# Kernel tuning notes

Hardware: AMD Instinct MI355X
Metric: run time of the kernel (lower is better)

Reference implementation:

```python
import jax, jax.numpy as jnp
import numpy as np

EPS = 1e-5

def _bn(x, gamma, beta):
    # x: [B, N, C]; training-mode BatchNorm1d over (B, N)
    mu = jnp.mean(x, axis=(0, 1))
    var = jnp.var(x, axis=(0, 1))
    return (x - mu) * jax.lax.rsqrt(var + EPS) * gamma + beta


def setup_inputs() -> dict:
    key = jax.random.key(0)
    ks = jax.random.split(key, 32)
    B, N = 16, 8192
    enc_dim, mem_dim = 1024, 1024
    feat_dim = enc_dim + mem_dim  # 2048
    n_points = 2048
    s = 0.02
    d = {
        'partial': jax.random.normal(ks[0], (B, N, 3), jnp.float32),
        # first_conv: Conv1d(3,128,1) + BN(128) + ReLU + Conv1d(128,256,1)
        'W1': jax.random.normal(ks[1], (128, 3), jnp.float32) * s,
        'b1': jnp.zeros((128,), jnp.float32),
        'g1': jnp.ones((128,), jnp.float32),
        'be1': jnp.zeros((128,), jnp.float32),
        'W2': jax.random.normal(ks[2], (256, 128), jnp.float32) * s,
        'b2': jnp.zeros((256,), jnp.float32),
        # second_conv: Conv1d(512,512,1) + BN(512) + ReLU + Conv1d(512,enc_dim,1)
        'W3': jax.random.normal(ks[3], (512, 512), jnp.float32) * s,
        'b3': jnp.zeros((512,), jnp.float32),
        'g2': jnp.ones((512,), jnp.float32),
        'be2': jnp.zeros((512,), jnp.float32),
        'W4': jax.random.normal(ks[4], (enc_dim, 512), jnp.float32) * s,
        'b4': jnp.zeros((enc_dim,), jnp.float32),
        # MemoryModule gates: Linear(enc_dim, mem_dim) x4 + memory param
        'Wf': jax.random.normal(ks[5], (mem_dim, enc_dim), jnp.float32) * s,
        'bf': jnp.zeros((mem_dim,), jnp.float32),
        'Wi': jax.random.normal(ks[6], (mem_dim, enc_dim), jnp.float32) * s,
        'bi': jnp.zeros((mem_dim,), jnp.float32),
        'Wo': jax.random.normal(ks[7], (mem_dim, enc_dim), jnp.float32) * s,
        'bo': jnp.zeros((mem_dim,), jnp.float32),
        'Wc': jax.random.normal(ks[8], (mem_dim, enc_dim), jnp.float32) * s,
        'bc': jnp.zeros((mem_dim,), jnp.float32),
        'mem': jax.random.normal(ks[9], (1, mem_dim), jnp.float32),
        # Decoder MLP: feat_dim->2048->2048->2048->3*n_points
        'D1w': jax.random.normal(ks[10], (2048, feat_dim), jnp.float32) * s,
        'D1b': jnp.zeros((2048,), jnp.float32),
        'D2w': jax.random.normal(ks[11], (2048, 2048), jnp.float32) * s,
        'D2b': jnp.zeros((2048,), jnp.float32),
        'D3w': jax.random.normal(ks[12], (2048, 2048), jnp.float32) * s,
        'D3b': jnp.zeros((2048,), jnp.float32),
        'D4w': jax.random.normal(ks[13], (3 * n_points, 2048), jnp.float32) * s,
        'D4b': jnp.zeros((3 * n_points,), jnp.float32),
    }
    return d


def reference(partial, W1, b1, g1, be1, W2, b2, W3, b3, g2, be2, W4, b4,
              Wf, bf, Wi, bi, Wo, bo, Wc, bc, mem,
              D1w, D1b, D2w, D2b, D3w, D3b, D4w, D4b):
    B, N, _ = partial.shape
    # --- Encoder first_conv (pointwise convs == per-point linear) ---
    f = jnp.einsum('bnc,dc->bnd', partial, W1) + b1          # [B,N,128]
    f = jax.nn.relu(_bn(f, g1, be1))
    f = jnp.einsum('bnc,dc->bnd', f, W2) + b2                # [B,N,256]
    fg = jnp.max(f, axis=1, keepdims=True)                   # [B,1,256]
    f = jnp.concatenate([jnp.broadcast_to(fg, (B, N, 256)), f], axis=-1)  # [B,N,512]
    # --- second_conv ---
    f = jnp.einsum('bnc,dc->bnd', f, W3) + b3                # [B,N,512]
    f = jax.nn.relu(_bn(f, g2, be2))
    f = jnp.einsum('bnc,dc->bnd', f, W4) + b4                # [B,N,enc_dim]
    feat_global = jnp.max(f, axis=1)                         # [B,enc_dim]
    # --- MemoryModule (flag=False: memory not updated) ---
    fgate = jax.nn.sigmoid(feat_global @ Wf.T + bf)
    igate = jax.nn.sigmoid(feat_global @ Wi.T + bi)
    ogate = jax.nn.sigmoid(feat_global @ Wo.T + bo)
    cand = jnp.tanh(feat_global @ Wc.T + bc)
    mem_b = jnp.broadcast_to(mem, fgate.shape)
    h = ogate * jnp.tanh(fgate * mem_b + igate * cand)       # [B,mem_dim]
    feat = jnp.concatenate([feat_global, h], axis=1)         # [B,feat_dim]
    # --- Decoder MLP ---
    z = jax.nn.relu(feat @ D1w.T + D1b)
    z = jax.nn.relu(z @ D2w.T + D2b)
    z = jax.nn.relu(z @ D3w.T + D3b)
    z = z @ D4w.T + D4b                                      # [B, 3*n_points]
    return z.reshape(B, -1, 3)
```

## Files before the change

kernel.cpp:

```cpp
#include <hip/hip_runtime.h>
#include <hip/hip_bf16.h>

typedef __bf16 v8bf __attribute__((ext_vector_type(8)));
typedef float  v4f  __attribute__((ext_vector_type(4)));

#define NPTS (16*8192)
#define RPB  8192

#define GLOAD_LDS16(g, l) __builtin_amdgcn_global_load_lds( \
    (const __attribute__((address_space(1))) void*)(g), \
    (__attribute__((address_space(3))) void*)(l), 16, 0, 0)

__device__ __forceinline__ unsigned fenc(float x){
    unsigned u = __float_as_uint(x);
    return (u & 0x80000000u) ? ~u : (u | 0x80000000u);
}
__device__ __forceinline__ float fdec(unsigned u){
    return __uint_as_float((u & 0x80000000u) ? (u ^ 0x80000000u) : ~u);
}

__device__ __forceinline__ v8bf bn_relu8(v8bf v, float4 s0, float4 s1, float4 h0, float4 h1){
    v8bf r;
    r[0] = (__bf16)fmaxf(fmaf((float)v[0], s0.x, h0.x), 0.f);
    r[1] = (__bf16)fmaxf(fmaf((float)v[1], s0.y, h0.y), 0.f);
    r[2] = (__bf16)fmaxf(fmaf((float)v[2], s0.z, h0.z), 0.f);
    r[3] = (__bf16)fmaxf(fmaf((float)v[3], s0.w, h0.w), 0.f);
    r[4] = (__bf16)fmaxf(fmaf((float)v[4], s1.x, h1.x), 0.f);
    r[5] = (__bf16)fmaxf(fmaf((float)v[5], s1.y, h1.y), 0.f);
    r[6] = (__bf16)fmaxf(fmaf((float)v[6], s1.z, h1.z), 0.f);
    r[7] = (__bf16)fmaxf(fmaf((float)v[7], s1.w, h1.w), 0.f);
    return r;
}

__global__ __launch_bounds__(256) void stats1_k(const float* __restrict__ P,
        const float* __restrict__ W1, const float* __restrict__ b1,
        float* __restrict__ gsum, float* __restrict__ gsumsq)
{
    int tid = threadIdx.x;
    int c = tid & 127, half = tid >> 7;
    float w0 = W1[c*3+0], w1 = W1[c*3+1], w2 = W1[c*3+2], bb = b1[c];
    float s = 0.f, s2 = 0.f;
    int base = blockIdx.x * 512 + half;
    for (int i = 0; i < 256; ++i) {
        int p = base + i*2;
        float x = P[p*3+0], y = P[p*3+1], z = P[p*3+2];
        float v = fmaf(w0,x, fmaf(w1,y, fmaf(w2,z, bb)));
        s += v; s2 = fmaf(v,v,s2);
    }
    __shared__ float ls[256], lq[256];
    ls[tid] = s; lq[tid] = s2;
    __syncthreads();
    if (half == 0) {
        atomicAdd(&gsum[c],   s  + ls[tid+128]);
        atomicAdd(&gsumsq[c], s2 + lq[tid+128]);
    }
}

__global__ void finalize_k(const float* __restrict__ gsum, const float* __restrict__ gsumsq,
        const float* __restrict__ gamma, const float* __restrict__ beta,
        float* __restrict__ scale, float* __restrict__ shift, int C, float invn)
{
    int c = blockIdx.x*blockDim.x + threadIdx.x;
    if (c >= C) return;
    float m   = gsum[c]*invn;
    float var = fmaxf(gsumsq[c]*invn - m*m, 0.f);
    float rs  = rsqrtf(var + 1e-5f);
    float sc  = gamma[c]*rs;
    scale[c] = sc;
    shift[c] = beta[c] - m*sc;
}

__global__ __launch_bounds__(256) void apply1_k(const float* __restrict__ P,
        const float* __restrict__ W1, const float* __restrict__ b1,
        const float* __restrict__ sc, const float* __restrict__ sh,
        __bf16* __restrict__ out)
{
    int tid = threadIdx.x;
    int c = tid & 127, ph = tid >> 7;
    float w0 = W1[c*3+0], w1 = W1[c*3+1], w2 = W1[c*3+2], bb = b1[c];
    float a = sc[c], b_ = sh[c];
    int base = blockIdx.x * 16 + ph;
    #pragma unroll
    for (int i = 0; i < 8; ++i) {
        int p = base + i*2;
        float x = P[p*3+0], y = P[p*3+1], z = P[p*3+2];
        float v = fmaf(w0,x, fmaf(w1,y, fmaf(w2,z, bb)));
        v = fmaxf(fmaf(v, a, b_), 0.f);
        out[(size_t)p*128 + c] = (__bf16)v;
    }
}

__global__ void cvt_k(const float* __restrict__ src, __bf16* __restrict__ dst,
                      int rows, int cols, int sstride, int coff)
{
    int i = blockIdx.x*256 + threadIdx.x;
    if (i >= rows*cols) return;
    int r = i / cols, c = i - r*cols;
    dst[i] = (__bf16)src[(size_t)r*sstride + coff + c];
}

template<bool STORE, bool DOMAX, bool STATS, bool BNA, int LOGNB>
__global__ __launch_bounds__(256, 2) void gemm_k(
        const __bf16* __restrict__ A, const __bf16* __restrict__ Bw,
        int K, int Nw,
        const float* __restrict__ bias, int bias_bstride,
        __bf16* __restrict__ Cout, unsigned* __restrict__ maxenc,
        float* __restrict__ gsum, float* __restrict__ gsq,
        const float* __restrict__ scA, const float* __restrict__ shA)
{
    __shared__ __bf16 As[128*64];
    __shared__ __bf16 Bs[256*64];
    __shared__ float lstat[2][2][256];

    const int tid  = threadIdx.x;
    const int lane = tid & 63;
    const int wave = tid >> 6;
    const int wr = wave >> 1, wc = wave & 1;
    const int nwg   = (int)gridDim.x;
    const int chunk = nwg >> 3;
    const int bi    = (int)blockIdx.x;
    const int li    = (bi & 7) * chunk + (bi >> 3);
    const int m0    = (li >> LOGNB) * 128;
    const int n0    = (li & ((1 << LOGNB) - 1)) * 256;
    const int srow = tid >> 3, sslot = tid & 7;
    const int lrow  = lane >> 3;
    const int swz   = ((lane & 7) ^ lrow) * 8;

    v4f acc[4][8];
    #pragma unroll
    for (int i=0;i<4;i++)
      #pragma unroll
      for (int j=0;j<8;j++) acc[i][j] = (v4f)(0.0f);

    v8bf ra[4];
    auto loadA_bn = [&](int kb){
        int kk = kb + sslot*8;
        float4 s0 = *(const float4*)(scA + kk);
        float4 s1 = *(const float4*)(scA + kk + 4);
        float4 h0 = *(const float4*)(shA + kk);
        float4 h1 = *(const float4*)(shA + kk + 4);
        #pragma unroll
        for (int i=0;i<4;i++){
            int r = i*32 + srow;
            v8bf v = *(const v8bf*)(A + (size_t)(m0+r)*K + kb + sslot*8);
            ra[i] = bn_relu8(v, s0, s1, h0, h1);
        }
    };
    auto stageB = [&](int kb){
        #pragma unroll
        for (int j=0;j<8;j++){
            int r0 = (wave*8 + j)*8;
            GLOAD_LDS16(Bw + (size_t)(n0 + r0 + lrow)*K + kb + swz, &Bs[r0*64]);
        }
    };
    auto stageA = [&](int kb){
        #pragma unroll
        for (int j=0;j<4;j++){
            int r0 = (wave*4 + j)*8;
            GLOAD_LDS16(A + (size_t)(m0 + r0 + lrow)*K + kb + swz, &As[r0*64]);
        }
    };

    if constexpr (BNA) loadA_bn(0);

    for (int k0 = 0; k0 < K; k0 += 64) {
        __syncthreads();
        stageB(k0);
        if constexpr (BNA) {
            #pragma unroll
            for (int i=0;i<4;i++){
                int r = i*32 + srow;
                *(v8bf*)(&As[r*64 + ((sslot ^ (r & 7))<<3)]) = ra[i];
            }
        } else {
            stageA(k0);
        }
        __syncthreads();
        if constexpr (BNA) { if (k0 + 64 < K) loadA_bn(k0 + 64); }
        #pragma unroll
        for (int kk = 0; kk < 2; ++kk) {
            v8bf af[4], bfr[8];
            #pragma unroll
            for (int i=0;i<4;i++){
                int arow = wr*64 + i*16 + (lane & 15);
                int sg = kk*4 + (lane >> 4);
                af[i] = *(const v8bf*)(&As[arow*64 + ((sg ^ (arow & 7))<<3)]);
            }
            #pragma unroll
            for (int j=0;j<8;j++){
                int brow = wc*128 + j*16 + (lane & 15);
                int sg = kk*4 + (lane >> 4);
                bfr[j] = *(const v8bf*)(&Bs[brow*64 + ((sg ^ (brow & 7))<<3)]);
            }
            #pragma unroll
            for (int i=0;i<4;i++)
              #pragma unroll
              for (int j=0;j<8;j++)
                acc[i][j] = __builtin_amdgcn_mfma_f32_16x16x32_bf16(af[i], bfr[j], acc[i][j], 0,0,0);
        }
    }

    const int b = m0 / RPB;
    const float* brow_ = bias + (size_t)b * bias_bstride;
    float colmax[8], csum[8], csq[8];
    #pragma unroll
    for (int j=0;j<8;j++){ colmax[j] = -3.402823466e38f; csum[j]=0.f; csq[j]=0.f; }

    #pragma unroll
    for (int i=0;i<4;i++){
        int rbase = m0 + wr*64 + i*16 + ((lane>>4)<<2);
        #pragma unroll
        for (int j=0;j<8;j++){
            int col = n0 + wc*128 + j*16 + (lane & 15);
            float bv = brow_[col];
            #pragma unroll
            for (int q=0;q<4;q++){
                float v = acc[i][j][q] + bv;
                if constexpr (STORE) Cout[(size_t)(rbase+q)*Nw + col] = (__bf16)v;
                if constexpr (DOMAX) colmax[j] = fmaxf(colmax[j], v);
                if constexpr (STATS) { csum[j] += v; csq[j] = fmaf(v,v,csq[j]); }
            }
        }
    }
    if constexpr (DOMAX) {
        #pragma unroll
        for (int j=0;j<8;j++){
            float v = colmax[j];
            v = fmaxf(v, __shfl_xor(v, 16));
            v = fmaxf(v, __shfl_xor(v, 32));
            if (lane < 16) {
                int col = n0 + wc*128 + j*16 + lane;
                atomicMax(&maxenc[(size_t)b*Nw + col], fenc(v));
            }
        }
    }
    if constexpr (STATS) {
        #pragma unroll
        for (int j=0;j<8;j++){
            float s = csum[j], q = csq[j];
            s += __shfl_xor(s, 16); s += __shfl_xor(s, 32);
            q += __shfl_xor(q, 16); q += __shfl_xor(q, 32);
            if (lane < 16) {
                int c = wc*128 + j*16 + lane;
                lstat[0][wr][c] = s;
                lstat[1][wr][c] = q;
            }
        }
        __syncthreads();
        if (tid < 256) {
            float s = lstat[0][0][tid] + lstat[0][1][tid];
            float q = lstat[1][0][tid] + lstat[1][1][tid];
            atomicAdd(&gsum[n0 + tid], s);
            atomicAdd(&gsq [n0 + tid], q);
        }
    }
}

__global__ __launch_bounds__(256) void bias3_k(const unsigned* __restrict__ fge,
        const float* __restrict__ W3, const float* __restrict__ b3,
        float* __restrict__ bias3)
{
    int b = blockIdx.x, tid = threadIdx.x;
    __shared__ float fg[256];
    fg[tid] = fdec(fge[b*256 + tid]);
    __syncthreads();
    for (int d = tid; d < 512; d += 256) {
        const float* wrow = W3 + (size_t)d*512;
        float s = b3[d];
        for (int c = 0; c < 256; c += 4) {
            s = fmaf(fg[c+0], wrow[c+0], s);
            s = fmaf(fg[c+1], wrow[c+1], s);
            s = fmaf(fg[c+2], wrow[c+2], s);
            s = fmaf(fg[c+3], wrow[c+3], s);
        }
        bias3[b*512 + d] = s;
    }
}

__global__ void decode_k(const unsigned* __restrict__ enc, float* __restrict__ feat)
{
    int i = blockIdx.x*256 + threadIdx.x;
    int b = i >> 10, c = i & 1023;
    feat[(size_t)b*2048 + c] = fdec(enc[i]);
}

__global__ __launch_bounds__(256) void gates_k(
        const float* __restrict__ Wf, const float* __restrict__ bfv,
        const float* __restrict__ Wi, const float* __restrict__ biv,
        const float* __restrict__ Wo, const float* __restrict__ bov,
        const float* __restrict__ Wc, const float* __restrict__ bcv,
        const float* __restrict__ memv, float* __restrict__ feat)
{
    int tid = threadIdx.x;
    int b = tid & 15;
    int j = blockIdx.x*16 + (tid >> 4);
    const float* x  = feat + (size_t)b*2048;
    const float* rf = Wf + (size_t)j*1024;
    const float* ri = Wi + (size_t)j*1024;
    const float* ro = Wo + (size_t)j*1024;
    const float* rc = Wc + (size_t)j*1024;
    float sf = bfv[j], si = biv[j], so = bov[j], scn = bcv[j];
    for (int c = 0; c < 1024; c += 4) {
        float4 xv = *(const float4*)(x + c);
        float4 a  = *(const float4*)(rf + c);
        sf = fmaf(xv.x,a.x, fmaf(xv.y,a.y, fmaf(xv.z,a.z, fmaf(xv.w,a.w, sf))));
        float4 bq = *(const float4*)(ri + c);
        si = fmaf(xv.x,bq.x, fmaf(xv.y,bq.y, fmaf(xv.z,bq.z, fmaf(xv.w,bq.w, si))));
        float4 cq = *(const float4*)(ro + c);
        so = fmaf(xv.x,cq.x, fmaf(xv.y,cq.y, fmaf(xv.z,cq.z, fmaf(xv.w,cq.w, so))));
        float4 dq = *(const float4*)(rc + c);
        scn= fmaf(xv.x,dq.x, fmaf(xv.y,dq.y, fmaf(xv.z,dq.z, fmaf(xv.w,dq.w, scn))));
    }
    float fg = 1.f/(1.f + expf(-sf));
    float ig = 1.f/(1.f + expf(-si));
    float og = 1.f/(1.f + expf(-so));
    float cd = tanhf(scn);
    float h  = og * tanhf(fmaf(fg, memv[j], ig*cd));
    feat[(size_t)b*2048 + 1024 + j] = h;
}

template<bool RELU>
__global__ __launch_bounds__(256) void dec2_k(const float* __restrict__ in,
        const float* __restrict__ W, const float* __restrict__ bias,
        float* __restrict__ out, int N)
{
    __shared__ float xin[16*2048];
    int tid = threadIdx.x;
    int lane = tid & 63, wv = tid >> 6;
    #pragma unroll
    for (int j = 0; j < 32; ++j) {
        int blk = wv*32 + j;
        GLOAD_LDS16(in + blk*256 + lane*4, &xin[blk*256]);
    }
    __syncthreads();
    #pragma unroll
    for (int c = 0; c < 2; ++c) {
        int col = blockIdx.x*8 + wv*2 + c;
        const float* wrow = W + (size_t)col*2048;
        float s[16];
        #pragma unroll
        for (int b=0;b<16;b++) s[b]=0.f;
        #pragma unroll
        for (int it = 0; it < 8; ++it) {
            int k = it*256 + lane*4;
            float4 w4 = *(const float4*)(wrow + k);
            #pragma unroll
            for (int b=0;b<16;b++){
                const float* xb = &xin[b*2048 + k];
                s[b] = fmaf(w4.x, xb[0], fmaf(w4.y, xb[1], fmaf(w4.z, xb[2], fmaf(w4.w, xb[3], s[b]))));
            }
        }
        #pragma unroll
        for (int off=32; off; off>>=1){
            #pragma unroll
            for (int b=0;b<16;b++) s[b] += __shfl_xor(s[b], off);
        }
        if (lane == 0) {
            float bv = bias[col];
            #pragma unroll
            for (int b=0;b<16;b++){
                float v = s[b] + bv;
                if (RELU) v = fmaxf(v, 0.f);
                out[(size_t)b*N + col] = v;
            }
        }
    }
}

extern "C" void kernel_launch(void* const* d_in, const int* in_sizes, int n_in,
                              void* d_out, int out_size, void* d_ws, size_t ws_size,
                              hipStream_t stream)
{
    (void)in_sizes; (void)n_in; (void)out_size; (void)ws_size;
    const float* partial = (const float*)d_in[0];
    const float* W1 = (const float*)d_in[1];
    const float* b1 = (const float*)d_in[2];
    const float* g1 = (const float*)d_in[3];
    const float* be1= (const float*)d_in[4];
    const float* W2 = (const float*)d_in[5];
    const float* b2 = (const float*)d_in[6];
    const float* W3 = (const float*)d_in[7];
    const float* b3 = (const float*)d_in[8];
    const float* g2 = (const float*)d_in[9];
    const float* be2= (const float*)d_in[10];
    const float* W4 = (const float*)d_in[11];
    const float* b4 = (const float*)d_in[12];
    const float* Wf = (const float*)d_in[13];
    const float* bfv= (const float*)d_in[14];
    const float* Wi = (const float*)d_in[15];
    const float* biv= (const float*)d_in[16];
    const float* Wo = (const float*)d_in[17];
    const float* bov= (const float*)d_in[18];
    const float* Wc = (const float*)d_in[19];
    const float* bcv= (const float*)d_in[20];
    const float* memv=(const float*)d_in[21];
    const float* D1w= (const float*)d_in[22];
    const float* D1b= (const float*)d_in[23];
    const float* D2w= (const float*)d_in[24];
    const float* D2b= (const float*)d_in[25];
    const float* D3w= (const float*)d_in[26];
    const float* D3b= (const float*)d_in[27];
    const float* D4w= (const float*)d_in[28];
    const float* D4b= (const float*)d_in[29];

    char* w = (char*)d_ws;
    size_t off = 0;
    auto alloc = [&](size_t bytes) -> void* {
        void* p = w + off; off += (bytes + 255) & ~(size_t)255; return p;
    };
    __bf16* y1bn = (__bf16*)alloc((size_t)NPTS*128*2);
    __bf16* f2   = (__bf16*)alloc((size_t)NPTS*256*2);
    __bf16* y3   = (__bf16*)alloc((size_t)NPTS*512*2);
    __bf16* W2b  = (__bf16*)alloc(256*128*2);
    __bf16* W3bb = (__bf16*)alloc(512*256*2);
    __bf16* W4b  = (__bf16*)alloc(1024*512*2);
    char* accbase = (char*)(w + off);
    float* gsum1    = (float*)alloc(128*4);
    float* gsumsq1  = (float*)alloc(128*4);
    float* gsum3    = (float*)alloc(512*4);
    float* gsumsq3  = (float*)alloc(512*4);
    unsigned* fg_enc    = (unsigned*)alloc(16*256*4);
    unsigned* featg_enc = (unsigned*)alloc(16*1024*4);
    size_t accbytes = (size_t)((w + off) - accbase);
    float* scale1 = (float*)alloc(128*4);
    float* shift1 = (float*)alloc(128*4);
    float* scale3 = (float*)alloc(512*4);
    float* shift3 = (float*)alloc(512*4);
    float* bias3  = (float*)alloc(16*512*4);
    float* feat   = (float*)alloc(16*2048*4);
    float* z1     = (float*)alloc(16*2048*4);
    float* z2     = (float*)alloc(16*2048*4);
    float* z3     = (float*)alloc(16*2048*4);

    hipMemsetAsync(accbase, 0, accbytes, stream);

    cvt_k<<<dim3(128), 256, 0, stream>>>(W2, W2b, 256, 128, 128, 0);
    cvt_k<<<dim3(512), 256, 0, stream>>>(W3, W3bb, 512, 256, 512, 256);
    cvt_k<<<dim3(2048),256, 0, stream>>>(W4, W4b, 1024, 512, 512, 0);

    stats1_k<<<dim3(256), 256, 0, stream>>>(partial, W1, b1, gsum1, gsumsq1);
    finalize_k<<<dim3(1), 128, 0, stream>>>(gsum1, gsumsq1, g1, be1, scale1, shift1, 128, 1.f/NPTS);
    apply1_k<<<dim3(8192), 256, 0, stream>>>(partial, W1, b1, scale1, shift1, y1bn);

    gemm_k<true,true,false,false,0><<<dim3(1024), 256, 0, stream>>>(
        y1bn, W2b, 128, 256, b2, 0, f2, fg_enc, nullptr, nullptr, nullptr, nullptr);

    bias3_k<<<dim3(16), 256, 0, stream>>>(fg_enc, W3, b3, bias3);

    gemm_k<true,false,true,false,1><<<dim3(2048), 256, 0, stream>>>(
        f2, W3bb, 256, 512, bias3, 512, y3, nullptr, gsum3, gsumsq3, nullptr, nullptr);

    finalize_k<<<dim3(2), 256, 0, stream>>>(gsum3, gsumsq3, g2, be2, scale3, shift3, 512, 1.f/NPTS);

    gemm_k<false,true,false,true,2><<<dim3(4096), 256, 0, stream>>>(
        y3, W4b, 512, 1024, b4, 0, nullptr, featg_enc, nullptr, nullptr, scale3, shift3);

    decode_k<<<dim3(64), 256, 0, stream>>>(featg_enc, feat);
    gates_k<<<dim3(64), 256, 0, stream>>>(Wf,bfv, Wi,biv, Wo,bov, Wc,bcv, memv, feat);

    dec2_k<true ><<<dim3(256), 256, 0, stream>>>(feat, D1w, D1b, z1, 2048);
    dec2_k<true ><<<dim3(256), 256, 0, stream>>>(z1,   D2w, D2b, z2, 2048);
    dec2_k<true ><<<dim3(256), 256, 0, stream>>>(z2,   D3w, D3b, z3, 2048);
    dec2_k<false><<<dim3(768), 256, 0, stream>>>(z3,   D4w, D4b, (float*)d_out, 6144);
}
```

Measured before the change: 478.6 us.

## Fuse first conv+BN+ReLU into GEMM A-load and merge small launch kernels

The first pointwise conv with BatchNorm and ReLU is now computed on the fly inside the W2 GEMM's A-tile load from the raw 3-channel points. This removes the apply1 kernel and the 32 MB bf16 y1bn intermediate it wrote and the GEMM then read back. The three weight-conversion kernels are merged into one launch, and the decode of the max-encoded features is folded into the gates kernel. In exchange, each GEMM thread now does extra scalar loads and FMAs for W1 and the points on every A tile, which adds register pressure.

```diff
diff --git a/kernel.cpp b/kernel.cpp
--- a/kernel.cpp
+++ b/kernel.cpp
@@ -70,43 +70,34 @@
     shift[c] = beta[c] - m*sc;
 }
 
-__global__ __launch_bounds__(256) void apply1_k(const float* __restrict__ P,
-        const float* __restrict__ W1, const float* __restrict__ b1,
-        const float* __restrict__ sc, const float* __restrict__ sh,
-        __bf16* __restrict__ out)
-{
-    int tid = threadIdx.x;
-    int c = tid & 127, ph = tid >> 7;
-    float w0 = W1[c*3+0], w1 = W1[c*3+1], w2 = W1[c*3+2], bb = b1[c];
-    float a = sc[c], b_ = sh[c];
-    int base = blockIdx.x * 16 + ph;
-    #pragma unroll
-    for (int i = 0; i < 8; ++i) {
-        int p = base + i*2;
-        float x = P[p*3+0], y = P[p*3+1], z = P[p*3+2];
-        float v = fmaf(w0,x, fmaf(w1,y, fmaf(w2,z, bb)));
-        v = fmaxf(fmaf(v, a, b_), 0.f);
-        out[(size_t)p*128 + c] = (__bf16)v;
-    }
-}
-
-__global__ void cvt_k(const float* __restrict__ src, __bf16* __restrict__ dst,
-                      int rows, int cols, int sstride, int coff)
+__global__ void cvt3_k(const float* __restrict__ W2, const float* __restrict__ W3,
+                       const float* __restrict__ W4,
+                       __bf16* __restrict__ W2b, __bf16* __restrict__ W3bb,
+                       __bf16* __restrict__ W4b)
 {
     int i = blockIdx.x*256 + threadIdx.x;
-    if (i >= rows*cols) return;
-    int r = i / cols, c = i - r*cols;
-    dst[i] = (__bf16)src[(size_t)r*sstride + coff + c];
-}
-
-template<bool STORE, bool DOMAX, bool STATS, bool BNA, int LOGNB>
+    if (i < 32768) {
+        W2b[i] = (__bf16)W2[i];
+    } else if (i < 32768 + 131072) {
+        int k = i - 32768;
+        int r = k >> 8, c = k & 255;
+        W3bb[k] = (__bf16)W3[(size_t)r*512 + 256 + c];
+    } else if (i < 32768 + 131072 + 524288) {
+        int k = i - 163840;
+        W4b[k] = (__bf16)W4[k];
+    }
+}
+
+template<bool STORE, bool DOMAX, bool STATS, int BNMODE, int LOGNB>
 __global__ __launch_bounds__(256, 2) void gemm_k(
         const __bf16* __restrict__ A, const __bf16* __restrict__ Bw,
         int K, int Nw,
         const float* __restrict__ bias, int bias_bstride,
         __bf16* __restrict__ Cout, unsigned* __restrict__ maxenc,
         float* __restrict__ gsum, float* __restrict__ gsq,
-        const float* __restrict__ scA, const float* __restrict__ shA)
+        const float* __restrict__ scA, const float* __restrict__ shA,
+        const float* __restrict__ P3, const float* __restrict__ W1,
+        const float* __restrict__ b1)
 {
     __shared__ __bf16 As[128*64];
     __shared__ __bf16 Bs[256*64];
@@ -133,17 +124,44 @@
       for (int j=0;j<8;j++) acc[i][j] = (v4f)(0.0f);
 
     v8bf ra[4];
-    auto loadA_bn = [&](int kb){
+    auto loadA_pre = [&](int kb){
         int kk = kb + sslot*8;
         float4 s0 = *(const float4*)(scA + kk);
         float4 s1 = *(const float4*)(scA + kk + 4);
         float4 h0 = *(const float4*)(shA + kk);
         float4 h1 = *(const float4*)(shA + kk + 4);
-        #pragma unroll
-        for (int i=0;i<4;i++){
-            int r = i*32 + srow;
-            v8bf v = *(const v8bf*)(A + (size_t)(m0+r)*K + kb + sslot*8);
-            ra[i] = bn_relu8(v, s0, s1, h0, h1);
+        if constexpr (BNMODE == 1) {
+            #pragma unroll
+            for (int i=0;i<4;i++){
+                int r = i*32 + srow;
+                v8bf v = *(const v8bf*)(A + (size_t)(m0+r)*K + kb + sslot*8);
+                ra[i] = bn_relu8(v, s0, s1, h0, h1);
+            }
+        } else if constexpr (BNMODE == 2) {
+            float wv0[8], wv1[8], wv2[8], bb[8];
+            #pragma unroll
+            for (int e=0;e<8;e++){
+                wv0[e] = W1[(kk+e)*3+0];
+                wv1[e] = W1[(kk+e)*3+1];
+                wv2[e] = W1[(kk+e)*3+2];
+                bb[e]  = b1[kk+e];
+            }
+            float sarr[8] = {s0.x,s0.y,s0.z,s0.w,s1.x,s1.y,s1.z,s1.w};
+            float harr[8] = {h0.x,h0.y,h0.z,h0.w,h1.x,h1.y,h1.z,h1.w};
+            #pragma unroll
+            for (int i=0;i<4;i++){
+                int r = i*32 + srow;
+                const float* pp = P3 + (size_t)(m0+r)*3;
+                float x = pp[0], y = pp[1], z = pp[2];
+                v8bf v;
+                #pragma unroll
+                for (int e=0;e<8;e++){
+                    float t = fmaf(wv0[e],x, fmaf(wv1[e],y, fmaf(wv2[e],z, bb[e])));
+                    t = fmaxf(fmaf(t, sarr[e], harr[e]), 0.f);
+                    v[e] = (__bf16)t;
+                }
+                ra[i] = v;
+            }
         }
     };
     auto stageB = [&](int kb){
@@ -161,12 +179,12 @@
         }
     };
 
-    if constexpr (BNA) loadA_bn(0);
+    if constexpr (BNMODE != 0) loadA_pre(0);
 
     for (int k0 = 0; k0 < K; k0 += 64) {
         __syncthreads();
         stageB(k0);
-        if constexpr (BNA) {
+        if constexpr (BNMODE != 0) {
             #pragma unroll
             for (int i=0;i<4;i++){
                 int r = i*32 + srow;
@@ -176,7 +194,7 @@
             stageA(k0);
         }
         __syncthreads();
-        if constexpr (BNA) { if (k0 + 64 < K) loadA_bn(k0 + 64); }
+        if constexpr (BNMODE != 0) { if (k0 + 64 < K) loadA_pre(k0 + 64); }
         #pragma unroll
         for (int kk = 0; kk < 2; ++kk) {
             v8bf af[4], bfr[8];
@@ -277,14 +295,7 @@
     }
 }
 
-__global__ void decode_k(const unsigned* __restrict__ enc, float* __restrict__ feat)
-{
-    int i = blockIdx.x*256 + threadIdx.x;
-    int b = i >> 10, c = i & 1023;
-    feat[(size_t)b*2048 + c] = fdec(enc[i]);
-}
-
-__global__ __launch_bounds__(256) void gates_k(
+__global__ __launch_bounds__(256) void gates2_k(const unsigned* __restrict__ enc,
         const float* __restrict__ Wf, const float* __restrict__ bfv,
         const float* __restrict__ Wi, const float* __restrict__ biv,
         const float* __restrict__ Wo, const float* __restrict__ bov,
@@ -294,14 +305,15 @@
     int tid = threadIdx.x;
     int b = tid & 15;
     int j = blockIdx.x*16 + (tid >> 4);
-    const float* x  = feat + (size_t)b*2048;
+    const unsigned* xe = enc + (size_t)b*1024;
     const float* rf = Wf + (size_t)j*1024;
     const float* ri = Wi + (size_t)j*1024;
     const float* ro = Wo + (size_t)j*1024;
     const float* rc = Wc + (size_t)j*1024;
     float sf = bfv[j], si = biv[j], so = bov[j], scn = bcv[j];
     for (int c = 0; c < 1024; c += 4) {
-        float4 xv = *(const float4*)(x + c);
+        uint4 u = *(const uint4*)(xe + c);
+        float4 xv = { fdec(u.x), fdec(u.y), fdec(u.z), fdec(u.w) };
         float4 a  = *(const float4*)(rf + c);
         sf = fmaf(xv.x,a.x, fmaf(xv.y,a.y, fmaf(xv.z,a.z, fmaf(xv.w,a.w, sf))));
         float4 bq = *(const float4*)(ri + c);
@@ -316,6 +328,7 @@
     float og = 1.f/(1.f + expf(-so));
     float cd = tanhf(scn);
     float h  = og * tanhf(fmaf(fg, memv[j], ig*cd));
+    feat[(size_t)b*2048 + j]        = fdec(enc[(size_t)b*1024 + j]);
     feat[(size_t)b*2048 + 1024 + j] = h;
 }
 
@@ -408,7 +421,6 @@
     auto alloc = [&](size_t bytes) -> void* {
         void* p = w + off; off += (bytes + 255) & ~(size_t)255; return p;
     };
-    __bf16* y1bn = (__bf16*)alloc((size_t)NPTS*128*2);
     __bf16* f2   = (__bf16*)alloc((size_t)NPTS*256*2);
     __bf16* y3   = (__bf16*)alloc((size_t)NPTS*512*2);
     __bf16* W2b  = (__bf16*)alloc(256*128*2);
@@ -434,29 +446,28 @@
 
     hipMemsetAsync(accbase, 0, accbytes, stream);
 
-    cvt_k<<<dim3(128), 256, 0, stream>>>(W2, W2b, 256, 128, 128, 0);
-    cvt_k<<<dim3(512), 256, 0, stream>>>(W3, W3bb, 512, 256, 512, 256);
-    cvt_k<<<dim3(2048),256, 0, stream>>>(W4, W4b, 1024, 512, 512, 0);
+    cvt3_k<<<dim3(2688), 256, 0, stream>>>(W2, W3, W4, W2b, W3bb, W4b);
 
     stats1_k<<<dim3(256), 256, 0, stream>>>(partial, W1, b1, gsum1, gsumsq1);
     finalize_k<<<dim3(1), 128, 0, stream>>>(gsum1, gsumsq1, g1, be1, scale1, shift1, 128, 1.f/NPTS);
-    apply1_k<<<dim3(8192), 256, 0, stream>>>(partial, W1, b1, scale1, shift1, y1bn);
-
-    gemm_k<true,true,false,false,0><<<dim3(1024), 256, 0, stream>>>(
-        y1bn, W2b, 128, 256, b2, 0, f2, fg_enc, nullptr, nullptr, nullptr, nullptr);
+
+    gemm_k<true,true,false,2,0><<<dim3(1024), 256, 0, stream>>>(
+        nullptr, W2b, 128, 256, b2, 0, f2, fg_enc, nullptr, nullptr,
+        scale1, shift1, partial, W1, b1);
 
     bias3_k<<<dim3(16), 256, 0, stream>>>(fg_enc, W3, b3, bias3);
 
-    gemm_k<true,false,true,false,1><<<dim3(2048), 256, 0, stream>>>(
-        f2, W3bb, 256, 512, bias3, 512, y3, nullptr, gsum3, gsumsq3, nullptr, nullptr);
+    gemm_k<true,false,true,0,1><<<dim3(2048), 256, 0, stream>>>(
+        f2, W3bb, 256, 512, bias3, 512, y3, nullptr, gsum3, gsumsq3,
+        nullptr, nullptr, nullptr, nullptr, nullptr);
 
     finalize_k<<<dim3(2), 256, 0, stream>>>(gsum3, gsumsq3, g2, be2, scale3, shift3, 512, 1.f/NPTS);
 
-    gemm_k<false,true,false,true,2><<<dim3(4096), 256, 0, stream>>>(
-        y3, W4b, 512, 1024, b4, 0, nullptr, featg_enc, nullptr, nullptr, scale3, shift3);
-
-    decode_k<<<dim3(64), 256, 0, stream>>>(featg_enc, feat);
-    gates_k<<<dim3(64), 256, 0, stream>>>(Wf,bfv, Wi,biv, Wo,bov, Wc,bcv, memv, feat);
+    gemm_k<false,true,false,1,2><<<dim3(4096), 256, 0, stream>>>(
+        y3, W4b, 512, 1024, b4, 0, nullptr, featg_enc, nullptr, nullptr,
+        scale3, shift3, nullptr, nullptr, nullptr);
+
+    gates2_k<<<dim3(64), 256, 0, stream>>>(featg_enc, Wf,bfv, Wi,biv, Wo,bov, Wc,bcv, memv, feat);
 
     dec2_k<true ><<<dim3(256), 256, 0, stream>>>(feat, D1w, D1b, z1, 2048);
     dec2_k<true ><<<dim3(256), 256, 0, stream>>>(z1,   D2w, D2b, z2, 2048);
```

Measured after the change: 481.0 us. No clear change (+0.5%).
